# Performance work log

Hardware: AMD Instinct MI355X
Metric: run time of the kernel (lower is better)

Reference implementation:

```python
import jax, jax.numpy as jnp
import numpy as np

ATOM_DIMS = [119, 5, 12, 12, 10, 6, 6, 2, 2]  # OGB full_atom_feature_dims
N, E, D, H, L, C, G = 50000, 400000, 64, 4, 3, 10, 512
NEG_SLOPE = 0.2


def setup_inputs() -> dict:
    key = jax.random.key(0)
    ks = jax.random.split(key, 12)
    total_vocab = sum(ATOM_DIMS)  # 174
    inp = {
        "nodes_features": jax.random.randint(ks[0], (N, 9), 0, 2),
        "edges_connectivity": jax.random.randint(ks[1], (2, E), 0, N),
        "batch": jnp.sort(jax.random.randint(ks[2], (N,), 0, G)),
        "atom_emb": jax.random.normal(ks[3], (total_vocab, D), jnp.float32) * 0.1,
        # GATv2 per-layer params: lin_l (source), lin_r (target), attention vec, out bias
        "Wl": jax.random.normal(ks[4], (L, D, H * D), jnp.float32) * 0.05,
        "bl": jnp.zeros((L, H * D), jnp.float32),
        "Wr": jax.random.normal(ks[5], (L, D, H * D), jnp.float32) * 0.05,
        "br": jnp.zeros((L, H * D), jnp.float32),
        "att": jax.random.normal(ks[6], (L, H, D), jnp.float32) * 0.1,
        "gat_bias": jnp.zeros((L, D), jnp.float32),
        "Wc": jax.random.normal(ks[7], (D, C), jnp.float32) * 0.05,
        "bc": jnp.zeros((C,), jnp.float32),
    }
    return inp


def reference(nodes_features, edges_connectivity, batch, atom_emb,
              Wl, bl, Wr, br, att, gat_bias, Wc, bc):
    # --- AtomEncoder: sum of 9 categorical embeddings (tables concatenated) ---
    offsets = jnp.asarray(np.cumsum([0] + ATOM_DIMS[:-1]), dtype=nodes_features.dtype)
    x = atom_emb[nodes_features + offsets[None, :]].sum(axis=1)  # [N, D]

    # --- add self-loops (GATv2Conv default add_self_loops=True) ---
    loops = jnp.arange(N, dtype=edges_connectivity.dtype)
    src = jnp.concatenate([edges_connectivity[0], loops])  # [E+N]
    dst = jnp.concatenate([edges_connectivity[1], loops])

    for l in range(L):
        xl = (x @ Wl[l] + bl[l]).reshape(N, H, D)  # source transform
        xr = (x @ Wr[l] + br[l]).reshape(N, H, D)  # target transform
        m = jax.nn.leaky_relu(xl[src] + xr[dst], NEG_SLOPE)      # [E+N, H, D]
        e = jnp.einsum('ehd,hd->eh', m, att[l])                  # [E+N, H]
        # segment softmax over incoming edges of each target node
        emax = jax.ops.segment_max(e, dst, num_segments=N)       # [N, H]
        ea = jnp.exp(e - emax[dst])
        denom = jax.ops.segment_sum(ea, dst, num_segments=N)
        alpha = ea / denom[dst]                                  # [E+N, H]
        out = jax.ops.segment_sum(alpha[:, :, None] * xl[src], dst, num_segments=N)
        x = out.mean(axis=1) + gat_bias[l]                       # concat=False -> head mean
        if l < L - 1:
            x = jax.nn.gelu(x, approximate=False)                # nn.GELU()

    # --- global mean pool over graphs ---
    sums = jax.ops.segment_sum(x, batch, num_segments=G)         # [G, D]
    cnt = jax.ops.segment_sum(jnp.ones((N,), x.dtype), batch, num_segments=G)
    pooled = sums / jnp.maximum(cnt, 1.0)[:, None]

    return pooled @ Wc + bc                                      # [G, C]
```

## Files before the change

### kernel.cpp

```cpp
#include <hip/hip_runtime.h>
#include <hip/hip_fp16.h>
#include <math.h>

#define NEG_SLOPE 0.2f
#define LOG2E 1.44269504088896340736f

#if __has_builtin(__builtin_amdgcn_exp2f)
#define EXP2(x) __builtin_amdgcn_exp2f(x)
#else
#define EXP2(x) exp2f(x)
#endif

#define DPP_ADD(p, ctrl) \
    p += __int_as_float(__builtin_amdgcn_update_dpp(0, __float_as_int(p), ctrl, 0xf, 0xf, true))

typedef __fp16 half4v __attribute__((ext_vector_type(4)));
typedef __fp16 half2v __attribute__((ext_vector_type(2)));
typedef float  f32x4  __attribute__((ext_vector_type(4)));

__device__ __forceinline__ unsigned f2h2(float x, float y) {
    union { unsigned u; __half2 h; } r;
    r.h = __floats2half2_rn(x, y);
    return r.u;
}

#if __has_builtin(__builtin_amdgcn_fdot2)
#define FDOT2(a, b, c) __builtin_amdgcn_fdot2((a), (b), (c), false)
#else
__device__ __forceinline__ float FDOT2(half2v a, half2v b, float c) {
    return c + (float)a[0] * (float)b[0] + (float)a[1] * (float)b[1];
}
#endif

__global__ __launch_bounds__(256) void embed_kernel(
        const int* __restrict__ feat, const float* __restrict__ emb,
        const int* __restrict__ dstE, int* __restrict__ counts,
        __half* __restrict__ x, int N, int E) {
    int gid = blockIdx.x * 256 + threadIdx.x;
    if (gid < E) atomicAdd(&counts[dstE[gid]], 1);

    const int offs[9] = {0, 119, 124, 136, 148, 158, 164, 170, 172};
    int sub  = threadIdx.x >> 6;
    int lane = threadIdx.x & 63;
    int n = __builtin_amdgcn_readfirstlane(blockIdx.x * 4 + sub);
    if (n >= N) return;
    float s = 0.f;
#pragma unroll
    for (int j = 0; j < 9; ++j) {
        int idx = feat[n * 9 + j] + offs[j];
        s += emb[idx * 64 + lane];
    }
    x[(size_t)n * 64 + lane] = __float2half(s);
}

__global__ __launch_bounds__(256) void gemm_kernel(
        const __half* __restrict__ x,
        const float* __restrict__ Wl, const float* __restrict__ Wr,
        const float* __restrict__ bl, const float* __restrict__ br,
        __half* __restrict__ xl, __half* __restrict__ xr, int N) {
    int w    = threadIdx.x >> 6;
    int lane = threadIdx.x & 63;
    int lo   = lane & 15;
    int hi   = lane >> 4;
    const float* W    = blockIdx.y ? Wr : Wl;
    const float* bias = blockIdx.y ? br : bl;
    __half*      out  = blockIdx.y ? xr : xl;
    int wbase = w * 64;
    int r0    = blockIdx.x * 64;

    half4v aw[4][4];
    float4 bv[4];
#pragma unroll
    for (int mt = 0; mt < 4; ++mt) {
        int c = wbase + mt * 16 + lo;
#pragma unroll
        for (int kt = 0; kt < 4; ++kt) {
            int k = kt * 16 + hi * 4;
            float f0 = W[(size_t)(k + 0) * 256 + c];
            float f1 = W[(size_t)(k + 1) * 256 + c];
            float f2 = W[(size_t)(k + 2) * 256 + c];
            float f3 = W[(size_t)(k + 3) * 256 + c];
            half2v p0 = __builtin_amdgcn_cvt_pkrtz(f0, f1);
            half2v p1 = __builtin_amdgcn_cvt_pkrtz(f2, f3);
            aw[mt][kt][0] = p0[0]; aw[mt][kt][1] = p0[1];
            aw[mt][kt][2] = p1[0]; aw[mt][kt][3] = p1[1];
        }
        bv[mt] = *(const float4*)(bias + wbase + mt * 16 + hi * 4);
    }

    half4v xv[4][4];
#pragma unroll
    for (int nt = 0; nt < 4; ++nt) {
        int row = min(r0 + nt * 16 + lo, N - 1);
        const __half* p = x + (size_t)row * 64 + hi * 4;
#pragma unroll
        for (int kt = 0; kt < 4; ++kt)
            xv[nt][kt] = *(const half4v*)(p + kt * 16);
    }

    f32x4 acc[4][4];
#pragma unroll
    for (int mt = 0; mt < 4; ++mt)
#pragma unroll
        for (int nt = 0; nt < 4; ++nt)
            acc[mt][nt] = (f32x4){0.f, 0.f, 0.f, 0.f};

#pragma unroll
    for (int kt = 0; kt < 4; ++kt)
#pragma unroll
        for (int mt = 0; mt < 4; ++mt)
#pragma unroll
            for (int nt = 0; nt < 4; ++nt)
                acc[mt][nt] = __builtin_amdgcn_mfma_f32_16x16x16f16(
                    aw[mt][kt], xv[nt][kt], acc[mt][nt], 0, 0, 0);

#pragma unroll
    for (int nt = 0; nt < 4; ++nt) {
        int row = r0 + nt * 16 + lo;
        if (row < N) {
#pragma unroll
            for (int mt = 0; mt < 4; ++mt) {
                f32x4 a = acc[mt][nt];
                half2v p0 = __builtin_amdgcn_cvt_pkrtz(a[0] + bv[mt].x, a[1] + bv[mt].y);
                half2v p1 = __builtin_amdgcn_cvt_pkrtz(a[2] + bv[mt].z, a[3] + bv[mt].w);
                union { half2v h[2]; uint2 u; } st;
                st.h[0] = p0; st.h[1] = p1;
                int c = wbase + mt * 16 + hi * 4;
                *(uint2*)(out + (size_t)row * 256 + c) = st.u;
            }
        }
    }
}

__global__ void scan_block_kernel(const int* __restrict__ counts, int* __restrict__ excl,
                                  int* __restrict__ blockSums, int N) {
    __shared__ int lds[256];
    int b = blockIdx.x, t = threadIdx.x;
    int base = b * 1024 + t * 4;
    int v0 = (base + 0 < N) ? counts[base + 0] + 1 : 0;
    int v1 = (base + 1 < N) ? counts[base + 1] + 1 : 0;
    int v2 = (base + 2 < N) ? counts[base + 2] + 1 : 0;
    int v3 = (base + 3 < N) ? counts[base + 3] + 1 : 0;
    int s = v0 + v1 + v2 + v3;
    lds[t] = s;
    __syncthreads();
    for (int off = 1; off < 256; off <<= 1) {
        int add = (t >= off) ? lds[t - off] : 0;
        __syncthreads();
        lds[t] += add;
        __syncthreads();
    }
    int run = lds[t] - s;
    if (base + 0 < N) excl[base + 0] = run; run += v0;
    if (base + 1 < N) excl[base + 1] = run; run += v1;
    if (base + 2 < N) excl[base + 2] = run; run += v2;
    if (base + 3 < N) excl[base + 3] = run;
    if (t == 255) blockSums[b] = lds[255];
}

__global__ void finalize_kernel(int* __restrict__ csr_off, const int* __restrict__ blockSums,
                                int* __restrict__ cursor, int* __restrict__ csr_src,
                                int N, int total, int nb) {
    __shared__ int incl[64];
    __shared__ int excl[64];
    int t = threadIdx.x;
    if (t < 64) incl[t] = (t < nb) ? blockSums[t] : 0;
    __syncthreads();
    for (int off = 1; off < 64; off <<= 1) {
        int add = (t >= off && t < 64) ? incl[t - off] : 0;
        __syncthreads();
        if (t < 64) incl[t] += add;
        __syncthreads();
    }
    if (t < 64) excl[t] = t ? incl[t - 1] : 0;
    __syncthreads();

    int i = blockIdx.x * 256 + t;
    if (i < N) {
        int v = csr_off[i] + excl[i >> 10];
        csr_off[i] = v;
        csr_src[v] = i;
        cursor[i]  = v + 1;
    }
    if (i == 0) csr_off[N] = total;
}

__global__ void scatter_kernel(const int* __restrict__ src, const int* __restrict__ dst,
                               int* __restrict__ cursor, int* __restrict__ csr_src, int E) {
    int e = blockIdx.x * 256 + threadIdx.x;
    if (e < E) {
        int pos = atomicAdd(&cursor[dst[e]], 1);
        csr_src[pos] = src[e];
    }
}

__global__ __launch_bounds__(256) void agg_kernel(
        const __half* __restrict__ xl, const __half* __restrict__ xr,
        const int* __restrict__ csr_off, const int* __restrict__ csr_src,
        const float* __restrict__ att,
        const float* __restrict__ gbias,
        __half* __restrict__ xout, int N, int apply_gelu) {
    int wave = threadIdx.x >> 6;
    int lane = threadIdx.x & 63;
    int n = __builtin_amdgcn_readfirstlane(blockIdx.x * 4 + wave);
    if (n >= N) return;

    union HU { uint2 u; half2v h[2]; };

    float4 attf = ((const float4*)att)[lane];
    half2v att_lo = __builtin_amdgcn_cvt_pkrtz(attf.x * LOG2E, attf.y * LOG2E);
    half2v att_hi = __builtin_amdgcn_cvt_pkrtz(attf.z * LOG2E, attf.w * LOG2E);

    HU xru; xru.u = *(const uint2*)(xr + (size_t)n * 256 + lane * 4);
    half2v xr_lo = xru.h[0], xr_hi = xru.h[1];
    const half2v ns2 = {(__fp16)NEG_SLOPE, (__fp16)NEG_SLOPE};

    int beg  = csr_off[n];
    int end  = csr_off[n + 1];
    int m    = end - beg;
    int last = end - 1;

    const __half* __restrict__ xlp = xl + lane * 4;

    auto idx4 = [&](int pos) -> int4 {
        int4 v;
        v.x = csr_src[min(pos,     last)];
        v.y = csr_src[min(pos + 1, last)];
        v.z = csr_src[min(pos + 2, last)];
        v.w = csr_src[min(pos + 3, last)];
        return v;
    };
    auto rows4 = [&](const int4& iv, uint2& r0, uint2& r1, uint2& r2, uint2& r3) {
        r0 = *(const uint2*)(xlp + (size_t)iv.x * 256);
        r1 = *(const uint2*)(xlp + (size_t)iv.y * 256);
        r2 = *(const uint2*)(xlp + (size_t)iv.z * 256);
        r3 = *(const uint2*)(xlp + (size_t)iv.w * 256);
    };
    auto logit = [&](half2v lo, half2v hi) -> float {
        half2v s0 = lo + xr_lo;
        half2v s1 = hi + xr_hi;
        half2v t0 = __builtin_elementwise_max(s0, s0 * ns2);
        half2v t1 = __builtin_elementwise_max(s1, s1 * ns2);
        return FDOT2(t1, att_hi, FDOT2(t0, att_lo, 0.f));
    };

    float ax = 0.f, ay = 0.f, az = 0.f, aw = 0.f, denom = 0.f;

    auto compute4 = [&](const uint2& q0, const uint2& q1, const uint2& q2,
                        const uint2& q3, int kbase) {
        HU e0, e1, e2, e3;
        e0.u = q0; e1.u = q1; e2.u = q2; e3.u = q3;
        float p0 = logit(e0.h[0], e0.h[1]);
        float p1 = logit(e1.h[0], e1.h[1]);
        float p2 = logit(e2.h[0], e2.h[1]);
        float p3 = logit(e3.h[0], e3.h[1]);
        DPP_ADD(p0, 0xB1);  DPP_ADD(p1, 0xB1);  DPP_ADD(p2, 0xB1);  DPP_ADD(p3, 0xB1);
        DPP_ADD(p0, 0x4E);  DPP_ADD(p1, 0x4E);  DPP_ADD(p2, 0x4E);  DPP_ADD(p3, 0x4E);
        DPP_ADD(p0, 0x141); DPP_ADD(p1, 0x141); DPP_ADD(p2, 0x141); DPP_ADD(p3, 0x141);
        DPP_ADD(p0, 0x140); DPP_ADD(p1, 0x140); DPP_ADD(p2, 0x140); DPP_ADD(p3, 0x140);
        float w0 = EXP2(p0);
        float w1 = (kbase + 1 < m) ? EXP2(p1) : 0.f;
        float w2 = (kbase + 2 < m) ? EXP2(p2) : 0.f;
        float w3 = (kbase + 3 < m) ? EXP2(p3) : 0.f;
        denom += (w0 + w1) + (w2 + w3);
        ax += w0 * (float)e0.h[0][0] + w1 * (float)e1.h[0][0]
            + w2 * (float)e2.h[0][0] + w3 * (float)e3.h[0][0];
        ay += w0 * (float)e0.h[0][1] + w1 * (float)e1.h[0][1]
            + w2 * (float)e2.h[0][1] + w3 * (float)e3.h[0][1];
        az += w0 * (float)e0.h[1][0] + w1 * (float)e1.h[1][0]
            + w2 * (float)e2.h[1][0] + w3 * (float)e3.h[1][0];
        aw += w0 * (float)e0.h[1][1] + w1 * (float)e1.h[1][1]
            + w2 * (float)e2.h[1][1] + w3 * (float)e3.h[1][1];
    };

    uint2 a0, a1, a2, a3, b0, b1, b2, b3, c0, c1, c2, c3;
    rows4(idx4(beg), a0, a1, a2, a3);
    if (m <= 4) {
        compute4(a0, a1, a2, a3, 0);
    } else {
        rows4(idx4(beg + 4), b0, b1, b2, b3);
        if (m <= 8) {
            compute4(a0, a1, a2, a3, 0);
            compute4(b0, b1, b2, b3, 4);
        } else {
            rows4(idx4(beg + 8), c0, c1, c2, c3);
            int4 ja = idx4(beg + 12);
            int4 jb = idx4(beg + 16);
            int4 jc = idx4(beg + 20);
            int g = 0;
            while (true) {
                compute4(a0, a1, a2, a3, g);
                if (g + 4 >= m) break;
                rows4(ja, a0, a1, a2, a3);  ja = idx4(beg + g + 24);

                compute4(b0, b1, b2, b3, g + 4);
                if (g + 8 >= m) break;
                rows4(jb, b0, b1, b2, b3);  jb = idx4(beg + g + 28);

                compute4(c0, c1, c2, c3, g + 8);
                if (g + 12 >= m) break;
                rows4(jc, c0, c1, c2, c3);  jc = idx4(beg + g + 32);

                g += 12;
            }
        }
    }

    float inv = 1.f / denom;
    float rx = ax * inv, ry = ay * inv, rz = az * inv, rw = aw * inv;
    rx += __shfl_xor(rx, 16); rx += __shfl_xor(rx, 32);
    ry += __shfl_xor(ry, 16); ry += __shfl_xor(ry, 32);
    rz += __shfl_xor(rz, 16); rz += __shfl_xor(rz, 32);
    rw += __shfl_xor(rw, 16); rw += __shfl_xor(rw, 32);

    if (lane < 16) {
        int d0 = lane * 4;
        float4 bvv = *(const float4*)(gbias + d0);
        float ox = 0.25f * rx + bvv.x;
        float oy = 0.25f * ry + bvv.y;
        float oz = 0.25f * rz + bvv.z;
        float ow = 0.25f * rw + bvv.w;
        if (apply_gelu) {
            const float kk = 0.70710678118654752440f;
            ox = 0.5f * ox * (1.f + erff(ox * kk));
            oy = 0.5f * oy * (1.f + erff(oy * kk));
            oz = 0.5f * oz * (1.f + erff(oz * kk));
            ow = 0.5f * ow * (1.f + erff(ow * kk));
        }
        uint2 st = make_uint2(f2h2(ox, oy), f2h2(oz, ow));
        *(uint2*)(xout + (size_t)n * 64 + d0) = st;
    }
}

__global__ __launch_bounds__(256) void pool_kernel(
        const __half* __restrict__ x, const int* __restrict__ batch,
        const float* __restrict__ Wc, const float* __restrict__ bc,
        float* __restrict__ out, int N, int G) {
    __shared__ float part[4][64];
    __shared__ float pooled[64];
    int g = blockIdx.x, t = threadIdx.x;
    int sub = t >> 6, lane = t & 63;
    int lo = 0, hi = N;
    while (lo < hi) { int mid = (lo + hi) >> 1; if (batch[mid] < g) lo = mid + 1; else hi = mid; }
    int beg = lo;
    hi = N;
    while (lo < hi) { int mid = (lo + hi) >> 1; if (batch[mid] < g + 1) lo = mid + 1; else hi = mid; }
    int end = lo;

    float acc = 0.f;
    for (int n = beg + sub; n < end; n += 4) acc += __half2float(x[(size_t)n * 64 + lane]);
    part[sub][lane] = acc;
    __syncthreads();
    if (t < 64) {
        float s = (part[0][t] + part[1][t]) + (part[2][t] + part[3][t]);
        int cnt = end - beg;
        pooled[t] = (cnt > 0) ? s / (float)cnt : 0.f;
    }
    __syncthreads();
    if (t < 10) {
        float o = bc[t];
        for (int d = 0; d < 64; ++d) o += pooled[d] * Wc[d * 10 + t];
        out[(size_t)g * 10 + t] = o;
    }
}

extern "C" void kernel_launch(void* const* d_in, const int* in_sizes, int n_in,
                              void* d_out, int out_size, void* d_ws, size_t ws_size,
                              hipStream_t stream) {
    const int*   feat  = (const int*)d_in[0];
    const int*   edges = (const int*)d_in[1];
    const int*   batch = (const int*)d_in[2];
    const float* emb   = (const float*)d_in[3];
    const float* Wl    = (const float*)d_in[4];
    const float* bl    = (const float*)d_in[5];
    const float* Wr    = (const float*)d_in[6];
    const float* br    = (const float*)d_in[7];
    const float* att   = (const float*)d_in[8];
    const float* gb    = (const float*)d_in[9];
    const float* Wc    = (const float*)d_in[10];
    const float* bc    = (const float*)d_in[11];
    float* out = (float*)d_out;

    const int N = in_sizes[2];
    const int E = in_sizes[1] / 2;
    const int G = out_size / 10;

    char* ws = (char*)d_ws;
    size_t off = 0;
    auto alloc = [&](size_t bytes) -> char* {
        char* p = ws + off;
        off = (off + bytes + 255) & ~(size_t)255;
        return p;
    };
    __half* x         = (__half*)alloc((size_t)N * 64 * 2);
    __half* xl        = (__half*)alloc((size_t)N * 256 * 2);
    __half* xr        = (__half*)alloc((size_t)N * 256 * 2);
    int*    counts    = (int*)alloc((size_t)N * 4);
    int*    csr_off   = (int*)alloc((size_t)(N + 8) * 4);
    int*    cursor    = (int*)alloc((size_t)N * 4);
    int*    csr_src   = (int*)alloc((size_t)(E + N + 64) * 4);
    int*    blockSums = (int*)alloc(256 * 4);

    const int* srcv = edges;
    const int* dstv = edges + E;

    hipMemsetAsync(counts, 0, (size_t)N * 4, stream);
    hipLaunchKernelGGL(embed_kernel, dim3((N + 3) / 4), dim3(256), 0, stream,
                       feat, emb, dstv, counts, x, N, E);

    int nb = (N + 1023) / 1024;
    hipLaunchKernelGGL(scan_block_kernel, dim3(nb), dim3(256), 0, stream, counts, csr_off, blockSums, N);
    hipLaunchKernelGGL(finalize_kernel, dim3((N + 255) / 256), dim3(256), 0, stream,
                       csr_off, blockSums, cursor, csr_src, N, E + N, nb);
    hipLaunchKernelGGL(scatter_kernel, dim3((E + 255) / 256), dim3(256), 0, stream, srcv, dstv, cursor, csr_src, E);

    int nchunks = (N + 63) / 64;
    for (int l = 0; l < 3; ++l) {
        hipLaunchKernelGGL(gemm_kernel, dim3(nchunks, 2), dim3(256), 0, stream,
                           x, Wl + (size_t)l * 64 * 256, Wr + (size_t)l * 64 * 256,
                           bl + l * 256, br + l * 256, xl, xr, N);
        hipLaunchKernelGGL(agg_kernel, dim3((N + 3) / 4), dim3(256), 0, stream,
                           xl, xr, csr_off, csr_src, att + l * 256, gb + l * 64,
                           x, N, (l < 2) ? 1 : 0);
    }

    hipLaunchKernelGGL(pool_kernel, dim3(G), dim3(256), 0, stream, x, batch, Wc, bc, out, N, G);
}
```

Baseline: 361.7 us.

## Split each wave into two half-waves processing separate edges with 16-byte row loads

The aggregation kernel now has each 32-lane half of a wave handle a different group of four edges, with each lane loading 8 fp16 values (16 bytes) of a source row instead of 4. Per-edge logit reduction drops one DPP step, index fetches use a vectorized 16-byte load when in bounds, and the two halves are combined with a cross-half shuffle at the end. The intent is to double the edges in flight per wave and use wider gathers, cutting instruction and latency overhead per edge. In exchange it doubles per-lane register use for rows and accumulators and drops the three-deep prefetch pipeline to two, which may lower occupancy.

Measured after the change: 370.5 us. +2.4%, slower.

```diff
diff --git a/kernel.cpp b/kernel.cpp
--- a/kernel.cpp
+++ b/kernel.cpp
@@ -202,17 +202,22 @@
         __half* __restrict__ xout, int N, int apply_gelu) {
     int wave = threadIdx.x >> 6;
     int lane = threadIdx.x & 63;
+    int hf   = lane >> 5;
+    int sl   = lane & 31;
     int n = __builtin_amdgcn_readfirstlane(blockIdx.x * 4 + wave);
     if (n >= N) return;
 
-    union HU { uint2 u; half2v h[2]; };
-
-    float4 attf = ((const float4*)att)[lane];
-    half2v att_lo = __builtin_amdgcn_cvt_pkrtz(attf.x * LOG2E, attf.y * LOG2E);
-    half2v att_hi = __builtin_amdgcn_cvt_pkrtz(attf.z * LOG2E, attf.w * LOG2E);
-
-    HU xru; xru.u = *(const uint2*)(xr + (size_t)n * 256 + lane * 4);
-    half2v xr_lo = xru.h[0], xr_hi = xru.h[1];
+    union HU4 { uint4 u; half2v h[4]; };
+
+    float4 af0 = *(const float4*)(att + sl * 8);
+    float4 af1 = *(const float4*)(att + sl * 8 + 4);
+    half2v attp[4];
+    attp[0] = __builtin_amdgcn_cvt_pkrtz(af0.x * LOG2E, af0.y * LOG2E);
+    attp[1] = __builtin_amdgcn_cvt_pkrtz(af0.z * LOG2E, af0.w * LOG2E);
+    attp[2] = __builtin_amdgcn_cvt_pkrtz(af1.x * LOG2E, af1.y * LOG2E);
+    attp[3] = __builtin_amdgcn_cvt_pkrtz(af1.z * LOG2E, af1.w * LOG2E);
+
+    HU4 xru; xru.u = *(const uint4*)(xr + (size_t)n * 256 + sl * 8);
     const half2v ns2 = {(__fp16)NEG_SLOPE, (__fp16)NEG_SLOPE};
 
     int beg  = csr_off[n];
@@ -220,115 +225,118 @@
     int m    = end - beg;
     int last = end - 1;
 
-    const __half* __restrict__ xlp = xl + lane * 4;
-
-    auto idx4 = [&](int pos) -> int4 {
+    const __half* __restrict__ xlp = xl + sl * 8;
+
+    auto idx4h = [&](int pos) -> int4 {
+        int p = pos + (hf << 2);
+        if (p + 3 <= last) {
+            int4 v; __builtin_memcpy(&v, csr_src + p, 16); return v;
+        }
         int4 v;
-        v.x = csr_src[min(pos,     last)];
-        v.y = csr_src[min(pos + 1, last)];
-        v.z = csr_src[min(pos + 2, last)];
-        v.w = csr_src[min(pos + 3, last)];
+        v.x = csr_src[min(p,     last)];
+        v.y = csr_src[min(p + 1, last)];
+        v.z = csr_src[min(p + 2, last)];
+        v.w = csr_src[min(p + 3, last)];
         return v;
     };
-    auto rows4 = [&](const int4& iv, uint2& r0, uint2& r1, uint2& r2, uint2& r3) {
-        r0 = *(const uint2*)(xlp + (size_t)iv.x * 256);
-        r1 = *(const uint2*)(xlp + (size_t)iv.y * 256);
-        r2 = *(const uint2*)(xlp + (size_t)iv.z * 256);
-        r3 = *(const uint2*)(xlp + (size_t)iv.w * 256);
+    auto rows8 = [&](const int4& iv, uint4& r0, uint4& r1, uint4& r2, uint4& r3) {
+        r0 = *(const uint4*)(xlp + (size_t)iv.x * 256);
+        r1 = *(const uint4*)(xlp + (size_t)iv.y * 256);
+        r2 = *(const uint4*)(xlp + (size_t)iv.z * 256);
+        r3 = *(const uint4*)(xlp + (size_t)iv.w * 256);
     };
-    auto logit = [&](half2v lo, half2v hi) -> float {
-        half2v s0 = lo + xr_lo;
-        half2v s1 = hi + xr_hi;
-        half2v t0 = __builtin_elementwise_max(s0, s0 * ns2);
-        half2v t1 = __builtin_elementwise_max(s1, s1 * ns2);
-        return FDOT2(t1, att_hi, FDOT2(t0, att_lo, 0.f));
+    auto logit8 = [&](const HU4& e) -> float {
+        float a = 0.f;
+#pragma unroll
+        for (int q = 0; q < 4; ++q) {
+            half2v s = e.h[q] + xru.h[q];
+            half2v t = __builtin_elementwise_max(s, s * ns2);
+            a = FDOT2(t, attp[q], a);
+        }
+        return a;
     };
 
-    float ax = 0.f, ay = 0.f, az = 0.f, aw = 0.f, denom = 0.f;
-
-    auto compute4 = [&](const uint2& q0, const uint2& q1, const uint2& q2,
-                        const uint2& q3, int kbase) {
-        HU e0, e1, e2, e3;
+    float accd[8] = {0.f, 0.f, 0.f, 0.f, 0.f, 0.f, 0.f, 0.f};
+    float denom = 0.f;
+
+    auto compute8 = [&](const uint4& q0, const uint4& q1, const uint4& q2,
+                        const uint4& q3, int kbase) {
+        HU4 e0, e1, e2, e3;
         e0.u = q0; e1.u = q1; e2.u = q2; e3.u = q3;
-        float p0 = logit(e0.h[0], e0.h[1]);
-        float p1 = logit(e1.h[0], e1.h[1]);
-        float p2 = logit(e2.h[0], e2.h[1]);
-        float p3 = logit(e3.h[0], e3.h[1]);
+        float p0 = logit8(e0), p1 = logit8(e1), p2 = logit8(e2), p3 = logit8(e3);
         DPP_ADD(p0, 0xB1);  DPP_ADD(p1, 0xB1);  DPP_ADD(p2, 0xB1);  DPP_ADD(p3, 0xB1);
         DPP_ADD(p0, 0x4E);  DPP_ADD(p1, 0x4E);  DPP_ADD(p2, 0x4E);  DPP_ADD(p3, 0x4E);
         DPP_ADD(p0, 0x141); DPP_ADD(p1, 0x141); DPP_ADD(p2, 0x141); DPP_ADD(p3, 0x141);
-        DPP_ADD(p0, 0x140); DPP_ADD(p1, 0x140); DPP_ADD(p2, 0x140); DPP_ADD(p3, 0x140);
-        float w0 = EXP2(p0);
-        float w1 = (kbase + 1 < m) ? EXP2(p1) : 0.f;
-        float w2 = (kbase + 2 < m) ? EXP2(p2) : 0.f;
-        float w3 = (kbase + 3 < m) ? EXP2(p3) : 0.f;
+        int base = kbase + (hf << 2);
+        float w0 = (base     < m) ? EXP2(p0) : 0.f;
+        float w1 = (base + 1 < m) ? EXP2(p1) : 0.f;
+        float w2 = (base + 2 < m) ? EXP2(p2) : 0.f;
+        float w3 = (base + 3 < m) ? EXP2(p3) : 0.f;
         denom += (w0 + w1) + (w2 + w3);
-        ax += w0 * (float)e0.h[0][0] + w1 * (float)e1.h[0][0]
-            + w2 * (float)e2.h[0][0] + w3 * (float)e3.h[0][0];
-        ay += w0 * (float)e0.h[0][1] + w1 * (float)e1.h[0][1]
-            + w2 * (float)e2.h[0][1] + w3 * (float)e3.h[0][1];
-        az += w0 * (float)e0.h[1][0] + w1 * (float)e1.h[1][0]
-            + w2 * (float)e2.h[1][0] + w3 * (float)e3.h[1][0];
-        aw += w0 * (float)e0.h[1][1] + w1 * (float)e1.h[1][1]
-            + w2 * (float)e2.h[1][1] + w3 * (float)e3.h[1][1];
+#pragma unroll
+        for (int q = 0; q < 4; ++q) {
+            accd[2 * q]     += w0 * (float)e0.h[q][0] + w1 * (float)e1.h[q][0]
+                             + w2 * (float)e2.h[q][0] + w3 * (float)e3.h[q][0];
+            accd[2 * q + 1] += w0 * (float)e0.h[q][1] + w1 * (float)e1.h[q][1]
+                             + w2 * (float)e2.h[q][1] + w3 * (float)e3.h[q][1];
+        }
     };
 
-    uint2 a0, a1, a2, a3, b0, b1, b2, b3, c0, c1, c2, c3;
-    rows4(idx4(beg), a0, a1, a2, a3);
-    if (m <= 4) {
-        compute4(a0, a1, a2, a3, 0);
+    uint4 a0, a1, a2, a3, b0, b1, b2, b3;
+    if (m <= 8) {
+        rows8(idx4h(beg), a0, a1, a2, a3);
+        compute8(a0, a1, a2, a3, 0);
+    } else if (m <= 16) {
+        int4 i0 = idx4h(beg), i1 = idx4h(beg + 8);
+        rows8(i0, a0, a1, a2, a3);
+        rows8(i1, b0, b1, b2, b3);
+        compute8(a0, a1, a2, a3, 0);
+        compute8(b0, b1, b2, b3, 8);
     } else {
-        rows4(idx4(beg + 4), b0, b1, b2, b3);
-        if (m <= 8) {
-            compute4(a0, a1, a2, a3, 0);
-            compute4(b0, b1, b2, b3, 4);
-        } else {
-            rows4(idx4(beg + 8), c0, c1, c2, c3);
-            int4 ja = idx4(beg + 12);
-            int4 jb = idx4(beg + 16);
-            int4 jc = idx4(beg + 20);
-            int g = 0;
-            while (true) {
-                compute4(a0, a1, a2, a3, g);
-                if (g + 4 >= m) break;
-                rows4(ja, a0, a1, a2, a3);  ja = idx4(beg + g + 24);
-
-                compute4(b0, b1, b2, b3, g + 4);
-                if (g + 8 >= m) break;
-                rows4(jb, b0, b1, b2, b3);  jb = idx4(beg + g + 28);
-
-                compute4(c0, c1, c2, c3, g + 8);
-                if (g + 12 >= m) break;
-                rows4(jc, c0, c1, c2, c3);  jc = idx4(beg + g + 32);
-
-                g += 12;
-            }
-        }
-    }
+        rows8(idx4h(beg),     a0, a1, a2, a3);
+        rows8(idx4h(beg + 8), b0, b1, b2, b3);
+        int g = 0;
+        while (true) {
+            compute8(a0, a1, a2, a3, g);
+            if (g + 8 >= m) break;
+            if (g + 16 < m) rows8(idx4h(beg + g + 16), a0, a1, a2, a3);
+            compute8(b0, b1, b2, b3, g + 8);
+            if (g + 16 >= m) break;
+            if (g + 24 < m) rows8(idx4h(beg + g + 24), b0, b1, b2, b3);
+            g += 16;
+        }
+    }
+
+    denom += __shfl_xor(denom, 32);
+#pragma unroll
+    for (int q = 0; q < 8; ++q) accd[q] += __shfl_xor(accd[q], 32);
 
     float inv = 1.f / denom;
-    float rx = ax * inv, ry = ay * inv, rz = az * inv, rw = aw * inv;
-    rx += __shfl_xor(rx, 16); rx += __shfl_xor(rx, 32);
-    ry += __shfl_xor(ry, 16); ry += __shfl_xor(ry, 32);
-    rz += __shfl_xor(rz, 16); rz += __shfl_xor(rz, 32);
-    rw += __shfl_xor(rw, 16); rw += __shfl_xor(rw, 32);
-
-    if (lane < 16) {
-        int d0 = lane * 4;
-        float4 bvv = *(const float4*)(gbias + d0);
-        float ox = 0.25f * rx + bvv.x;
-        float oy = 0.25f * ry + bvv.y;
-        float oz = 0.25f * rz + bvv.z;
-        float ow = 0.25f * rw + bvv.w;
+#pragma unroll
+    for (int q = 0; q < 8; ++q) {
+        float r = accd[q] * inv;
+        r += __shfl_xor(r, 8);
+        r += __shfl_xor(r, 16);
+        accd[q] = r;
+    }
+
+    if (lane < 8) {
+        float4 bv0 = *(const float4*)(gbias + lane * 8);
+        float4 bv1 = *(const float4*)(gbias + lane * 8 + 4);
+        float o[8];
+        o[0] = 0.25f * accd[0] + bv0.x;  o[1] = 0.25f * accd[1] + bv0.y;
+        o[2] = 0.25f * accd[2] + bv0.z;  o[3] = 0.25f * accd[3] + bv0.w;
+        o[4] = 0.25f * accd[4] + bv1.x;  o[5] = 0.25f * accd[5] + bv1.y;
+        o[6] = 0.25f * accd[6] + bv1.z;  o[7] = 0.25f * accd[7] + bv1.w;
         if (apply_gelu) {
             const float kk = 0.70710678118654752440f;
-            ox = 0.5f * ox * (1.f + erff(ox * kk));
-            oy = 0.5f * oy * (1.f + erff(oy * kk));
-            oz = 0.5f * oz * (1.f + erff(oz * kk));
-            ow = 0.5f * ow * (1.f + erff(ow * kk));
-        }
-        uint2 st = make_uint2(f2h2(ox, oy), f2h2(oz, ow));
-        *(uint2*)(xout + (size_t)n * 64 + d0) = st;
+#pragma unroll
+            for (int q = 0; q < 8; ++q)
+                o[q] = 0.5f * o[q] * (1.f + erff(o[q] * kk));
+        }
+        uint4 st = make_uint4(f2h2(o[0], o[1]), f2h2(o[2], o[3]),
+                              f2h2(o[4], o[5]), f2h2(o[6], o[7]));
+        *(uint4*)(xout + (size_t)n * 64 + lane * 8) = st;
     }
 }
 
```
